# Kernel tuning notes

Measured on AMD Instinct MI355X. Metric: run time of the kernel, lower is better.

The kernel has to match this reference:

```python
import jax, jax.numpy as jnp
import numpy as np

L, B, T, C, H, V, BS = 4, 2, 1024, 768, 12, 50257, 1024


def _layernorm(x, g, b, eps=1e-5):
    m = jnp.mean(x, axis=-1, keepdims=True)
    v = jnp.mean(jnp.square(x - m), axis=-1, keepdims=True)
    return (x - m) * jax.lax.rsqrt(v + eps) * g + b


def setup_inputs() -> dict:
    key = jax.random.key(0)
    ks = jax.random.split(key, 8)
    s = 0.02
    return {
        "idx": jax.random.randint(ks[0], (B, T), 0, V),
        "wte": jax.random.normal(ks[1], (V, C), jnp.float32) * s,
        "wpe": jax.random.normal(ks[2], (BS, C), jnp.float32) * s,
        "ln1_g": jnp.ones((L, C), jnp.float32),
        "ln1_b": jnp.zeros((L, C), jnp.float32),
        "w_attn": jax.random.normal(ks[3], (L, C, 3 * C), jnp.float32) * s,
        "b_attn": jnp.zeros((L, 3 * C), jnp.float32),
        "w_ap": jax.random.normal(ks[4], (L, C, C), jnp.float32) * s,
        "b_ap": jnp.zeros((L, C), jnp.float32),
        "ln2_g": jnp.ones((L, C), jnp.float32),
        "ln2_b": jnp.zeros((L, C), jnp.float32),
        "w_fc": jax.random.normal(ks[5], (L, C, 4 * C), jnp.float32) * s,
        "b_fc": jnp.zeros((L, 4 * C), jnp.float32),
        "w_mp": jax.random.normal(ks[6], (L, 4 * C, C), jnp.float32) * s,
        "b_mp": jnp.zeros((L, C), jnp.float32),
        "lnf_g": jnp.ones((C,), jnp.float32),
        "lnf_b": jnp.zeros((C,), jnp.float32),
        "w_head": jax.random.normal(ks[7], (C, V), jnp.float32) * s,
    }


def _gpt_forward(idx, wte, wpe, ln1_g, ln1_b, w_attn, b_attn, w_ap, b_ap,
                 ln2_g, ln2_b, w_fc, b_fc, w_mp, b_mp, lnf_g, lnf_b, w_head):
    b, t = idx.shape
    hd = C // H
    mask = jnp.tril(jnp.ones((t, t), dtype=bool))  # causal mask
    x = wte[idx] + wpe[:t][None, :, :]  # [B,T,C], dropout p=0 -> identity

    def block(x, p):
        g1, b1, wa, ba, wp, bp, g2, b2, wf, bf, wm, bm = p
        h = _layernorm(x, g1, b1)
        qkv = h @ wa + ba  # [B,T,3C]
        q, k, v = jnp.split(qkv, 3, axis=-1)
        q = q.reshape(b, t, H, hd).transpose(0, 2, 1, 3)  # [B,H,T,hd]
        k = k.reshape(b, t, H, hd).transpose(0, 2, 1, 3)
        v = v.reshape(b, t, H, hd).transpose(0, 2, 1, 3)
        att = jnp.einsum('bhqd,bhkd->bhqk', q, k) * (1.0 / np.sqrt(hd))
        att = jnp.where(mask, att, -jnp.inf)
        att = jax.nn.softmax(att, axis=-1)
        y = jnp.einsum('bhqk,bhkd->bhqd', att, v)
        y = y.transpose(0, 2, 1, 3).reshape(b, t, C)
        x = x + (y @ wp + bp)
        h2 = _layernorm(x, g2, b2)
        x = x + (jax.nn.gelu(h2 @ wf + bf, approximate=False) @ wm + bm)
        return x, None

    layer_params = (ln1_g, ln1_b, w_attn, b_attn, w_ap, b_ap,
                    ln2_g, ln2_b, w_fc, b_fc, w_mp, b_mp)
    x, _ = jax.lax.scan(block, x, layer_params)
    x = _layernorm(x, lnf_g, lnf_b)
    return x @ w_head  # logits [B,T,V]


def reference(idx, wte, wpe, ln1_g, ln1_b, w_attn, b_attn, w_ap, b_ap,
              ln2_g, ln2_b, w_fc, b_fc, w_mp, b_mp, lnf_g, lnf_b, w_head):
    return _gpt_forward(idx, wte, wpe, ln1_g, ln1_b, w_attn, b_attn, w_ap,
                        b_ap, ln2_g, ln2_b, w_fc, b_fc, w_mp, b_mp,
                        lnf_g, lnf_b, w_head)
```

## Files before the change

kernel.cpp:

```cpp
#include <hip/hip_runtime.h>
#include <hip/hip_bf16.h>
#include <cstdint>
#include <cstddef>


typedef __bf16 bf16x8 __attribute__((ext_vector_type(8)));
typedef float floatx4 __attribute__((ext_vector_type(4)));

__device__ inline float bf2f(uint16_t h) {
    union { uint32_t u; float f; } x; x.u = ((uint32_t)h) << 16; return x.f;
}
__device__ inline uint16_t f2bf(float f) {
    union { float f; uint32_t u; } x; x.f = f;
    uint32_t u = x.u;
    uint32_t r = (u + 0x7fffu + ((u >> 16) & 1u)) >> 16;
    return (uint16_t)r;
}

__global__ void transpose_cvt(const float* __restrict__ in, uint16_t* __restrict__ out,
                              int K, int N, size_t in_lstride, size_t out_lstride) {
    __shared__ float tile[32][33];
    in  += (size_t)blockIdx.z * in_lstride;
    out += (size_t)blockIdx.z * out_lstride;
    int n0 = blockIdx.x * 32, k0 = blockIdx.y * 32;
    int tx = threadIdx.x, ty = threadIdx.y;
#pragma unroll
    for (int i = 0; i < 4; ++i) {
        int k = k0 + ty + i * 8;
        int n = n0 + tx;
        tile[ty + i * 8][tx] = (n < N) ? in[(size_t)k * N + n] : 0.f;
    }
    __syncthreads();
#pragma unroll
    for (int i = 0; i < 4; ++i) {
        int n = n0 + ty + i * 8;
        int k = k0 + tx;
        out[(size_t)n * K + k] = f2bf(tile[tx][ty + i * 8]);
    }
}

__global__ void embed_kernel(const int* __restrict__ idx, const float* __restrict__ wte,
                             const float* __restrict__ wpe, float* __restrict__ x) {
    int tid = blockIdx.x * 256 + threadIdx.x;
    int row = tid / 768, c = tid - row * 768;
    int t = row & 1023;
    int tok = idx[row];
    x[tid] = wte[(size_t)tok * 768 + c] + wpe[(size_t)t * 768 + c];
}

__global__ __launch_bounds__(256) void ln_kernel(const float* __restrict__ x,
                                                 const float* __restrict__ g,
                                                 const float* __restrict__ beta,
                                                 uint16_t* __restrict__ out) {
    int row = blockIdx.x;
    int t = threadIdx.x;
    int w = t >> 6, lane = t & 63;
    const float* xr = x + (size_t)row * 768;
    float v0 = xr[t], v1 = xr[t + 256], v2 = xr[t + 512];
    float s = v0 + v1 + v2;
    float s2 = v0 * v0 + v1 * v1 + v2 * v2;
#pragma unroll
    for (int mk = 32; mk >= 1; mk >>= 1) {
        s += __shfl_xor(s, mk, 64);
        s2 += __shfl_xor(s2, mk, 64);
    }
    __shared__ float rs[4], rq[4];
    if (lane == 0) { rs[w] = s; rq[w] = s2; }
    __syncthreads();
    float S = rs[0] + rs[1] + rs[2] + rs[3];
    float S2 = rq[0] + rq[1] + rq[2] + rq[3];
    float mean = S * (1.f / 768.f);
    float var = S2 * (1.f / 768.f) - mean * mean;
    float rinv = rsqrtf(var + 1e-5f);
    uint16_t* orow = out + (size_t)row * 768;
    orow[t]       = f2bf((v0 - mean) * rinv * g[t]       + beta[t]);
    orow[t + 256] = f2bf((v1 - mean) * rinv * g[t + 256] + beta[t + 256]);
    orow[t + 512] = f2bf((v2 - mean) * rinv * g[t + 512] + beta[t + 512]);
}

enum { EPI_BF16 = 0, EPI_GELU = 1, EPI_RESID = 2, EPI_F32 = 3 };

template <int EPI>
__global__ __launch_bounds__(256, 2)
void gemm128(const uint16_t* __restrict__ A, const uint16_t* __restrict__ Bt,
             const float* __restrict__ bias, uint16_t* __restrict__ Cbf,
             float* __restrict__ Cf, int M, int N, int K, int Nstore) {
    __shared__ __align__(16) uint16_t As[128][40];
    __shared__ __align__(16) uint16_t Bs[128][40];
    const int bm = blockIdx.y, bn = blockIdx.x;
    const int t = threadIdx.x;
    const int w = t >> 6, lane = t & 63;
    const int wy = w >> 1, wx = w & 1;
    const int q = lane >> 4, r = lane & 15;

    floatx4 acc[4][4];
#pragma unroll
    for (int i = 0; i < 4; ++i)
#pragma unroll
        for (int j = 0; j < 4; ++j)
            acc[i][j] = (floatx4){0.f, 0.f, 0.f, 0.f};

    const size_t abase = (size_t)(bm * 128) * K;
    const size_t bbase = (size_t)(bn * 128) * K;

    for (int k0 = 0; k0 < K; k0 += 32) {
#pragma unroll
        for (int s = 0; s < 2; ++s) {
            int c = t + s * 256;
            int row = c >> 2, col = (c & 3) * 8;
            *(uint4*)&As[row][col] = *(const uint4*)(A + abase + (size_t)row * K + k0 + col);
            *(uint4*)&Bs[row][col] = *(const uint4*)(Bt + bbase + (size_t)row * K + k0 + col);
        }
        __syncthreads();
        bf16x8 fa[4], fb[4];
#pragma unroll
        for (int i = 0; i < 4; ++i) fa[i] = *(const bf16x8*)&As[wy * 64 + i * 16 + r][q * 8];
#pragma unroll
        for (int j = 0; j < 4; ++j) fb[j] = *(const bf16x8*)&Bs[wx * 64 + j * 16 + r][q * 8];
#pragma unroll
        for (int i = 0; i < 4; ++i)
#pragma unroll
            for (int j = 0; j < 4; ++j)
                acc[i][j] = __builtin_amdgcn_mfma_f32_16x16x32_bf16(fa[i], fb[j], acc[i][j], 0, 0, 0);
        __syncthreads();
    }

#pragma unroll
    for (int i = 0; i < 4; ++i) {
#pragma unroll
        for (int j = 0; j < 4; ++j) {
#pragma unroll
            for (int e = 0; e < 4; ++e) {
                int m = bm * 128 + wy * 64 + i * 16 + q * 4 + e;
                int n = bn * 128 + wx * 64 + j * 16 + r;
                float v = acc[i][j][e];
                if (bias) v += bias[n];
                if (EPI == EPI_GELU) v = 0.5f * v * (1.f + erff(v * 0.70710678118f));
                if (EPI == EPI_BF16 || EPI == EPI_GELU) {
                    Cbf[(size_t)m * N + n] = f2bf(v);
                } else if (EPI == EPI_RESID) {
                    Cf[(size_t)m * N + n] += v;
                } else {
                    if (n < Nstore) Cf[(size_t)m * Nstore + n] = v;
                }
            }
        }
    }
}

__global__ __launch_bounds__(256) void fattn_kernel(const uint16_t* __restrict__ qkv,
                                                    uint16_t* __restrict__ y) {
    __shared__ __align__(16) uint16_t Ks[64][72];
    __shared__ __align__(16) uint16_t Vt[64][72];
    __shared__ __align__(16) uint16_t Pl[4][16][72];

    const int t = threadIdx.x;
    const int w = t >> 6, lane = t & 63;
    const int q = lane >> 4, r = lane & 15;
    const int bh = blockIdx.x;
    const int qb = 15 - blockIdx.y;
    const int b_ = bh / 12, h = bh - b_ * 12;
    const int qrow0 = qb * 64 + w * 16;

    bf16x8 fq0, fq1;
    {
        const uint16_t* qp = qkv + ((size_t)(b_ * 1024 + qrow0 + r)) * 2304 + h * 64 + q * 8;
        fq0 = *(const bf16x8*)qp;
        fq1 = *(const bf16x8*)(qp + 32);
    }

    floatx4 o[4];
    float m_[4], l_[4];
#pragma unroll
    for (int jt = 0; jt < 4; ++jt) o[jt] = (floatx4){0.f, 0.f, 0.f, 0.f};
#pragma unroll
    for (int e = 0; e < 4; ++e) { m_[e] = -INFINITY; l_[e] = 0.f; }

    for (int kb = 0; kb <= qb; ++kb) {
        const int kv0 = kb * 64;
#pragma unroll
        for (int s = 0; s < 2; ++s) {
            int c = t + s * 256;
            int row = c >> 3;
            int col = (c & 7) * 8;
            const uint16_t* kp = qkv + ((size_t)(b_ * 1024 + kv0 + row)) * 2304
                                 + 768 + h * 64 + col;
            *(uint4*)&Ks[row][col] = *(const uint4*)kp;
            uint16_t __attribute__((aligned(16))) tmp[8];
            *(uint4*)tmp = *(const uint4*)(kp + 768);
#pragma unroll
            for (int j0 = 0; j0 < 8; ++j0) {
                int j = (j0 + t) & 7;
                Vt[col + j][row] = tmp[j];
            }
        }
        __syncthreads();

        floatx4 s4[4];
#pragma unroll
        for (int j = 0; j < 4; ++j) s4[j] = (floatx4){0.f, 0.f, 0.f, 0.f};
#pragma unroll
        for (int ks = 0; ks < 2; ++ks) {
            bf16x8 fa = ks ? fq1 : fq0;
#pragma unroll
            for (int j = 0; j < 4; ++j) {
                bf16x8 fk = *(const bf16x8*)&Ks[j * 16 + r][ks * 32 + q * 8];
                s4[j] = __builtin_amdgcn_mfma_f32_16x16x32_bf16(fa, fk, s4[j], 0, 0, 0);
            }
        }

        const bool diag = (kb == qb);
#pragma unroll
        for (int e = 0; e < 4; ++e) {
            float v[4];
#pragma unroll
            for (int j = 0; j < 4; ++j) v[j] = s4[j][e] * 0.125f;
            if (diag) {
                int qi = w * 16 + q * 4 + e;
#pragma unroll
                for (int j = 0; j < 4; ++j)
                    if (j * 16 + r > qi) v[j] = -INFINITY;
            }
            float rm = fmaxf(fmaxf(v[0], v[1]), fmaxf(v[2], v[3]));
#pragma unroll
            for (int mk = 1; mk <= 8; mk <<= 1) rm = fmaxf(rm, __shfl_xor(rm, mk, 64));
            float mn = fmaxf(m_[e], rm);
            float al = __expf(m_[e] - mn);
            float p[4], rsum = 0.f;
#pragma unroll
            for (int j = 0; j < 4; ++j) { p[j] = __expf(v[j] - mn); rsum += p[j]; }
#pragma unroll
            for (int mk = 1; mk <= 8; mk <<= 1) rsum += __shfl_xor(rsum, mk, 64);
            l_[e] = l_[e] * al + rsum;
            m_[e] = mn;
#pragma unroll
            for (int jt = 0; jt < 4; ++jt) o[jt][e] *= al;
#pragma unroll
            for (int j = 0; j < 4; ++j) Pl[w][q * 4 + e][j * 16 + r] = f2bf(p[j]);
        }
        asm volatile("s_waitcnt lgkmcnt(0)" ::: "memory");

#pragma unroll
        for (int ks = 0; ks < 2; ++ks) {
            bf16x8 pa = *(const bf16x8*)&Pl[w][r][ks * 32 + q * 8];
#pragma unroll
            for (int jt = 0; jt < 4; ++jt) {
                bf16x8 vb = *(const bf16x8*)&Vt[jt * 16 + r][ks * 32 + q * 8];
                o[jt] = __builtin_amdgcn_mfma_f32_16x16x32_bf16(pa, vb, o[jt], 0, 0, 0);
            }
        }
        __syncthreads();
    }

    uint16_t* yrow = y + ((size_t)(b_ * 1024 + qrow0)) * 768 + h * 64;
#pragma unroll
    for (int e = 0; e < 4; ++e) {
        float inv = 1.f / l_[e];
        int qi = q * 4 + e;
#pragma unroll
        for (int jt = 0; jt < 4; ++jt)
            yrow[(size_t)qi * 768 + jt * 16 + r] = f2bf(o[jt][e] * inv);
    }
}

extern "C" void kernel_launch(void* const* d_in, const int* in_sizes, int n_in,
                              void* d_out, int out_size, void* d_ws, size_t ws_size,
                              hipStream_t stream) {
    (void)in_sizes; (void)n_in; (void)out_size; (void)ws_size;
    const int*   idx    = (const int*)  d_in[0];
    const float* wte    = (const float*)d_in[1];
    const float* wpe    = (const float*)d_in[2];
    const float* ln1_g  = (const float*)d_in[3];
    const float* ln1_b  = (const float*)d_in[4];
    const float* w_attn = (const float*)d_in[5];
    const float* b_attn = (const float*)d_in[6];
    const float* w_ap   = (const float*)d_in[7];
    const float* b_ap   = (const float*)d_in[8];
    const float* ln2_g  = (const float*)d_in[9];
    const float* ln2_b  = (const float*)d_in[10];
    const float* w_fc   = (const float*)d_in[11];
    const float* b_fc   = (const float*)d_in[12];
    const float* w_mp   = (const float*)d_in[13];
    const float* b_mp   = (const float*)d_in[14];
    const float* lnf_g  = (const float*)d_in[15];
    const float* lnf_b  = (const float*)d_in[16];
    const float* w_head = (const float*)d_in[17];
    float* out = (float*)d_out;

    char* p = (char*)d_ws;
    auto take = [&](size_t bytes) -> char* {
        char* r = p; p += (bytes + 255) & ~(size_t)255; return r;
    };
    float*    x     = (float*)   take((size_t)2048 * 768 * 4);
    uint16_t* h     = (uint16_t*)take((size_t)2048 * 768 * 2);
    uint16_t* qkv   = (uint16_t*)take((size_t)2048 * 2304 * 2);
    uint16_t* y     = (uint16_t*)take((size_t)2048 * 768 * 2);
    uint16_t* fca   = (uint16_t*)take((size_t)2048 * 3072 * 2);
    uint16_t* attnT = (uint16_t*)take((size_t)4 * 2304 * 768 * 2);
    uint16_t* apT   = (uint16_t*)take((size_t)4 * 768 * 768 * 2);
    uint16_t* fcT   = (uint16_t*)take((size_t)4 * 3072 * 768 * 2);
    uint16_t* mpT   = (uint16_t*)take((size_t)4 * 768 * 3072 * 2);
    uint16_t* headT = (uint16_t*)take((size_t)50304 * 768 * 2);

    dim3 tb(32, 8);
    transpose_cvt<<<dim3(2304 / 32, 768 / 32, 4), tb, 0, stream>>>(
        w_attn, attnT, 768, 2304, (size_t)768 * 2304, (size_t)2304 * 768);
    transpose_cvt<<<dim3(768 / 32, 768 / 32, 4), tb, 0, stream>>>(
        w_ap, apT, 768, 768, (size_t)768 * 768, (size_t)768 * 768);
    transpose_cvt<<<dim3(3072 / 32, 768 / 32, 4), tb, 0, stream>>>(
        w_fc, fcT, 768, 3072, (size_t)768 * 3072, (size_t)3072 * 768);
    transpose_cvt<<<dim3(768 / 32, 3072 / 32, 4), tb, 0, stream>>>(
        w_mp, mpT, 3072, 768, (size_t)3072 * 768, (size_t)768 * 3072);
    transpose_cvt<<<dim3(50304 / 32, 768 / 32, 1), tb, 0, stream>>>(
        w_head, headT, 768, 50257, 0, 0);

    embed_kernel<<<6144, 256, 0, stream>>>(idx, wte, wpe, x);

    for (int l = 0; l < 4; ++l) {
        ln_kernel<<<2048, 256, 0, stream>>>(x, ln1_g + l * 768, ln1_b + l * 768, h);
        gemm128<EPI_BF16><<<dim3(2304 / 128, 16), 256, 0, stream>>>(
            h, attnT + (size_t)l * 2304 * 768, b_attn + l * 2304, qkv, nullptr,
            2048, 2304, 768, 2304);
        fattn_kernel<<<dim3(24, 16), 256, 0, stream>>>(qkv, y);
        gemm128<EPI_RESID><<<dim3(768 / 128, 16), 256, 0, stream>>>(
            y, apT + (size_t)l * 768 * 768, b_ap + l * 768, nullptr, x,
            2048, 768, 768, 768);
        ln_kernel<<<2048, 256, 0, stream>>>(x, ln2_g + l * 768, ln2_b + l * 768, h);
        gemm128<EPI_GELU><<<dim3(3072 / 128, 16), 256, 0, stream>>>(
            h, fcT + (size_t)l * 3072 * 768, b_fc + l * 3072, fca, nullptr,
            2048, 3072, 768, 3072);
        gemm128<EPI_RESID><<<dim3(768 / 128, 16), 256, 0, stream>>>(
            fca, mpT + (size_t)l * 768 * 3072, b_mp + l * 768, nullptr, x,
            2048, 768, 3072, 768);
    }
    ln_kernel<<<2048, 256, 0, stream>>>(x, lnf_g, lnf_b, h);
    gemm128<EPI_F32><<<dim3(50304 / 128, 16), 256, 0, stream>>>(
        h, headT, nullptr, nullptr, out, 2048, 50304, 768, 50257);
}
```

Before: 2.001 ms.

## Use direct global-to-LDS loads, split-K residual GEMMs, and grouped block remapping

The GEMM now loads its A and B tiles straight into LDS with global_load_lds and drops the padded LDS rows. It also remaps block indices across 8 groups so co-scheduled blocks share tiles, intended for L2 reuse. The two residual projection GEMMs, which only have 96 blocks, are split along K into 2 and 4 slices that accumulate into x with atomicAdd, with the bias added only by the first slice, so more CUs are busy. The risks are LDS bank conflicts from the unpadded rows, extra atomic traffic, and nondeterministic float summation order.

```diff
diff --git a/kernel.cpp b/kernel.cpp
--- a/kernel.cpp
+++ b/kernel.cpp
@@ -15,6 +15,13 @@
     uint32_t u = x.u;
     uint32_t r = (u + 0x7fffu + ((u >> 16) & 1u)) >> 16;
     return (uint16_t)r;
+}
+
+__device__ inline void gload_lds16(const uint16_t* __restrict__ g, uint16_t* l) {
+    __builtin_amdgcn_global_load_lds(
+        (const __attribute__((address_space(1))) void*)(const void*)g,
+        (__attribute__((address_space(3))) void*)(void*)l,
+        16, 0, 0);
 }
 
 __global__ void transpose_cvt(const float* __restrict__ in, uint16_t* __restrict__ out,
@@ -85,14 +92,24 @@
 void gemm128(const uint16_t* __restrict__ A, const uint16_t* __restrict__ Bt,
              const float* __restrict__ bias, uint16_t* __restrict__ Cbf,
              float* __restrict__ Cf, int M, int N, int K, int Nstore) {
-    __shared__ __align__(16) uint16_t As[128][40];
-    __shared__ __align__(16) uint16_t Bs[128][40];
-    const int bm = blockIdx.y, bn = blockIdx.x;
+    __shared__ __align__(16) uint16_t As[128][32];
+    __shared__ __align__(16) uint16_t Bs[128][32];
     const int t = threadIdx.x;
     const int w = t >> 6, lane = t & 63;
     const int wy = w >> 1, wx = w & 1;
     const int q = lane >> 4, r = lane & 15;
 
+    const int nbn = gridDim.x;
+    const int flat = blockIdx.y * nbn + blockIdx.x;
+    const int per = (nbn * 16) >> 3;
+    const int virt = (flat & 7) * per + (flat >> 3);
+    const int bm = virt & 15;
+    const int bn = virt >> 4;
+
+    const int ksl = K / (int)gridDim.z;
+    const int k_beg = (int)blockIdx.z * ksl;
+    const int k_end = k_beg + ksl;
+
     floatx4 acc[4][4];
 #pragma unroll
     for (int i = 0; i < 4; ++i)
@@ -102,15 +119,17 @@
 
     const size_t abase = (size_t)(bm * 128) * K;
     const size_t bbase = (size_t)(bn * 128) * K;
-
-    for (int k0 = 0; k0 < K; k0 += 32) {
-#pragma unroll
-        for (int s = 0; s < 2; ++s) {
-            int c = t + s * 256;
-            int row = c >> 2, col = (c & 3) * 8;
-            *(uint4*)&As[row][col] = *(const uint4*)(A + abase + (size_t)row * K + k0 + col);
-            *(uint4*)&Bs[row][col] = *(const uint4*)(Bt + bbase + (size_t)row * K + k0 + col);
-        }
+    const int srow = lane >> 2;
+    const int scol = (lane & 3) * 8;
+
+    for (int k0 = k_beg; k0 < k_end; k0 += 32) {
+#pragma unroll
+        for (int c = 0; c < 2; ++c) {
+            int row = w * 32 + c * 16 + srow;
+            gload_lds16(A + abase + (size_t)row * K + k0 + scol, &As[w * 32 + c * 16][0]);
+            gload_lds16(Bt + bbase + (size_t)row * K + k0 + scol, &Bs[w * 32 + c * 16][0]);
+        }
+        asm volatile("s_waitcnt vmcnt(0)" ::: "memory");
         __syncthreads();
         bf16x8 fa[4], fb[4];
 #pragma unroll
@@ -134,12 +153,12 @@
                 int m = bm * 128 + wy * 64 + i * 16 + q * 4 + e;
                 int n = bn * 128 + wx * 64 + j * 16 + r;
                 float v = acc[i][j][e];
-                if (bias) v += bias[n];
+                if (bias && blockIdx.z == 0) v += bias[n];
                 if (EPI == EPI_GELU) v = 0.5f * v * (1.f + erff(v * 0.70710678118f));
                 if (EPI == EPI_BF16 || EPI == EPI_GELU) {
                     Cbf[(size_t)m * N + n] = f2bf(v);
                 } else if (EPI == EPI_RESID) {
-                    Cf[(size_t)m * N + n] += v;
+                    atomicAdd(&Cf[(size_t)m * N + n], v);
                 } else {
                     if (n < Nstore) Cf[(size_t)m * Nstore + n] = v;
                 }
@@ -322,14 +341,14 @@
             h, attnT + (size_t)l * 2304 * 768, b_attn + l * 2304, qkv, nullptr,
             2048, 2304, 768, 2304);
         fattn_kernel<<<dim3(24, 16), 256, 0, stream>>>(qkv, y);
-        gemm128<EPI_RESID><<<dim3(768 / 128, 16), 256, 0, stream>>>(
+        gemm128<EPI_RESID><<<dim3(768 / 128, 16, 2), 256, 0, stream>>>(
             y, apT + (size_t)l * 768 * 768, b_ap + l * 768, nullptr, x,
             2048, 768, 768, 768);
         ln_kernel<<<2048, 256, 0, stream>>>(x, ln2_g + l * 768, ln2_b + l * 768, h);
         gemm128<EPI_GELU><<<dim3(3072 / 128, 16), 256, 0, stream>>>(
             h, fcT + (size_t)l * 3072 * 768, b_fc + l * 3072, fca, nullptr,
             2048, 3072, 768, 3072);
-        gemm128<EPI_RESID><<<dim3(768 / 128, 16), 256, 0, stream>>>(
+        gemm128<EPI_RESID><<<dim3(768 / 128, 16, 4), 256, 0, stream>>>(
             fca, mpT + (size_t)l * 768 * 3072, b_mp + l * 768, nullptr, x,
             2048, 768, 3072, 768);
     }
```

New measurement: 1.808 ms. -9.6%, faster.
